# Kernel optimization log

Measured on AMD Instinct MI355X. Metric: run time of the kernel, lower is better.

## Reference

```python
import jax, jax.numpy as jnp
import numpy as np

S, B, D, H = 2048, 4, 1024, 16
HD = D // H  # 64
NEG = -1e9


def _rope_cache(seq_len, dim, base=10000.0):
    inv_freq = 1.0 / (base ** (jnp.arange(0, dim, 2, dtype=jnp.float32) / dim))
    pos = jnp.arange(seq_len, dtype=jnp.float32)
    freqs = jnp.einsum('i,j->ij', pos, inv_freq)          # [S, dim/2]
    emb = jnp.concatenate([freqs, freqs], axis=-1)         # [S, dim]
    return jnp.cos(emb)[None, None], jnp.sin(emb)[None, None]  # [1,1,S,dim]


def _apply_rotary(x, cos, sin):
    # rotated[..., ::2] = -x[..., 1::2]; rotated[..., 1::2] = x[..., ::2]
    x_even = x[..., ::2]
    x_odd = x[..., 1::2]
    rotated = jnp.stack([-x_odd, x_even], axis=-1).reshape(x.shape)
    return x * cos + rotated * sin


def setup_inputs() -> dict:
    key = jax.random.key(0)
    kx, kq, ko = jax.random.split(key, 3)
    x = jax.random.normal(kx, (S, B, D), dtype=jnp.float32)
    # additive causal mask, broadcastable over [B,H,S,S]
    causal = jnp.triu(jnp.full((S, S), NEG, dtype=jnp.float32), k=1)
    cos, sin = _rope_cache(S, HD)
    Wqkv = jax.random.normal(kq, (D, 3 * D), dtype=jnp.float32) * (D ** -0.5)
    Wout = jax.random.normal(ko, (D, D), dtype=jnp.float32) * (D ** -0.5)
    return {"x": x, "attn_mask": causal, "cos": cos, "sin": sin,
            "Wqkv": Wqkv, "Wout": Wout}


def reference(x, attn_mask, cos, sin, Wqkv, Wout):
    scale = 1.0 / jnp.sqrt(jnp.float32(HD))
    xb = jnp.swapaxes(x, 0, 1)                       # [B,S,D]
    qkv = jnp.einsum('bsd,de->bse', xb, Wqkv)        # [B,S,3D]
    q, k, v = jnp.split(qkv, 3, axis=-1)
    def heads(t):
        return t.reshape(B, S, H, HD).transpose(0, 2, 1, 3)  # [B,H,S,HD]
    q, k, v = heads(q), heads(k), heads(v)
    q = _apply_rotary(q, cos, sin)
    k = _apply_rotary(k, cos, sin)
    scores = jnp.einsum('bhsd,bhtd->bhst', q, k) * scale + attn_mask
    probs = jax.nn.softmax(scores, axis=-1)
    ctx = jnp.einsum('bhst,bhtd->bhsd', probs, v)
    ctx = ctx.transpose(0, 2, 1, 3).reshape(B, S, D)  # [B,S,D]
    out = jnp.einsum('bsd,de->bse', ctx, Wout)
    return jnp.swapaxes(out, 0, 1)                    # [S,B,D]
```

## Files before the change

kernel.cpp:

```cpp
#include <hip/hip_runtime.h>
#include <hip/hip_bf16.h>

#define S_LEN 2048
#define BATCH 4
#define DMODEL 1024
#define NHEAD 16
#define HDIM 64
#define E3 3072

typedef __bf16 bf16x8 __attribute__((ext_vector_type(8)));
typedef __bf16 bf16x4 __attribute__((ext_vector_type(4)));
typedef __bf16 bf16x2 __attribute__((ext_vector_type(2)));
typedef float f32x4 __attribute__((ext_vector_type(4)));

typedef const __attribute__((address_space(1))) void gvoid;
typedef __attribute__((address_space(3))) void lvoid;

__global__ void cast_f32_bf16(const float* __restrict__ src, __bf16* __restrict__ dst) {
    int i = (blockIdx.x * 256 + threadIdx.x) * 8;
    float4 a = *(const float4*)(src + i);
    float4 b = *(const float4*)(src + i + 4);
    bf16x8 v;
    v[0] = (__bf16)a.x; v[1] = (__bf16)a.y; v[2] = (__bf16)a.z; v[3] = (__bf16)a.w;
    v[4] = (__bf16)b.x; v[5] = (__bf16)b.y; v[6] = (__bf16)b.z; v[7] = (__bf16)b.w;
    *(bf16x8*)(dst + i) = v;
}

__global__ void transpose_f32_bf16(const float* __restrict__ src, __bf16* __restrict__ dst,
                                   int R, int C) {
    __shared__ float tile[32][33];
    int c0 = blockIdx.x * 32, r0 = blockIdx.y * 32;
    int tx = threadIdx.x, ty = threadIdx.y;
#pragma unroll
    for (int i = 0; i < 32; i += 8)
        tile[ty + i][tx] = src[(size_t)(r0 + ty + i) * C + c0 + tx];
    __syncthreads();
#pragma unroll
    for (int i = 0; i < 32; i += 8)
        dst[(size_t)(c0 + ty + i) * R + r0 + tx] = (__bf16)tile[tx][ty + i];
}

__global__ __launch_bounds__(256) void gemm_bt(
    const __bf16* __restrict__ A, const __bf16* __restrict__ BT, void* __restrict__ C,
    int K, int aSB, int aSS, int cSB, int cSS, int mode,
    const float* __restrict__ cosb, const float* __restrict__ sinb,
    __bf16* __restrict__ vtg) {
    __shared__ __bf16 lA[128 * 32];
    __shared__ __bf16 lB[128 * 32];

    const int tid = threadIdx.x;
    const int lane = tid & 63;
    const int quad = lane >> 4, l16 = lane & 15;
    const int wave = tid >> 6;
    const int wm = wave >> 1, wn = wave & 1;

    const int bid0 = blockIdx.y * gridDim.x + blockIdx.x;
    const int nwg = gridDim.x * gridDim.y;
    const int lid = (bid0 & 7) * (nwg >> 3) + (bid0 >> 3);
    const int bx = lid % gridDim.x;
    const int by = lid / gridDim.x;

    const int rm0 = by * 128;
    const int n0 = bx * 128;
    const int bb = rm0 / S_LEN;
    const int s0 = rm0 % S_LEN;

    const int lrow = lane >> 2;
    const int lch = (lane & 3) * 8;
    const int row0 = wave * 32;
    const __bf16* gA0 = A + (size_t)bb * aSB + (size_t)(s0 + row0 + lrow) * aSS + lch;
    const __bf16* gA1 = A + (size_t)bb * aSB + (size_t)(s0 + row0 + 16 + lrow) * aSS + lch;
    const __bf16* gB0 = BT + (size_t)(n0 + row0 + lrow) * K + lch;
    const __bf16* gB1 = BT + (size_t)(n0 + row0 + 16 + lrow) * K + lch;
    __bf16* ldsA0 = &lA[row0 * 32];
    __bf16* ldsA1 = &lA[(row0 + 16) * 32];
    __bf16* ldsB0 = &lB[row0 * 32];
    __bf16* ldsB1 = &lB[(row0 + 16) * 32];

    f32x4 acc[4][4];
#pragma unroll
    for (int i = 0; i < 4; i++)
#pragma unroll
        for (int j = 0; j < 4; j++) acc[i][j] = (f32x4){0.f, 0.f, 0.f, 0.f};

    for (int k0 = 0; k0 < K; k0 += 32) {
        __builtin_amdgcn_global_load_lds((gvoid*)(gA0 + k0), (lvoid*)ldsA0, 16, 0, 0);
        __builtin_amdgcn_global_load_lds((gvoid*)(gA1 + k0), (lvoid*)ldsA1, 16, 0, 0);
        __builtin_amdgcn_global_load_lds((gvoid*)(gB0 + k0), (lvoid*)ldsB0, 16, 0, 0);
        __builtin_amdgcn_global_load_lds((gvoid*)(gB1 + k0), (lvoid*)ldsB1, 16, 0, 0);
        __syncthreads();

        bf16x8 aF[4], bF[4];
#pragma unroll
        for (int i = 0; i < 4; i++) {
            aF[i] = *(const bf16x8*)&lA[(wm * 64 + i * 16 + l16) * 32 + quad * 8];
            bF[i] = *(const bf16x8*)&lB[(wn * 64 + i * 16 + l16) * 32 + quad * 8];
        }
#pragma unroll
        for (int i = 0; i < 4; i++)
#pragma unroll
            for (int j = 0; j < 4; j++)
                acc[i][j] = __builtin_amdgcn_mfma_f32_16x16x32_bf16(aF[i], bF[j], acc[i][j], 0, 0, 0);
        __syncthreads();
    }

    if (mode == 0) {
        if (n0 < 2048) {
#pragma unroll
            for (int i = 0; i < 4; i++) {
                const int rl = wm * 64 + i * 16 + quad * 4;
#pragma unroll
                for (int r = 0; r < 4; r++) {
                    const int s = s0 + rl + r;
                    const size_t rowOff = (size_t)bb * cSB + (size_t)s * cSS + n0 + wn * 64 + l16;
                    __bf16* cRow = (__bf16*)C + rowOff;
                    const float* cpr = cosb + s * HDIM;
                    const float* spr = sinb + s * HDIM;
#pragma unroll
                    for (int j = 0; j < 4; j++) {
                        float x = acc[i][j][r];
                        float y = __int_as_float(
                            __builtin_amdgcn_ds_swizzle(__float_as_int(x), 0x041F));
                        float c = cpr[j * 16 + l16];
                        float sn = spr[j * 16 + l16];
                        float out = (l16 & 1) ? fmaf(y, sn, x * c) : fmaf(-y, sn, x * c);
                        cRow[j * 16] = (__bf16)out;
                    }
                }
            }
        } else {
#pragma unroll
            for (int i = 0; i < 4; i++) {
                const int rl = wm * 64 + i * 16 + quad * 4;
#pragma unroll
                for (int j = 0; j < 4; j++) {
                    const int vcol = (n0 - 2048) + wn * 64 + j * 16 + l16;
                    const size_t vbase = ((size_t)(bb * 1024 + vcol)) * S_LEN + s0 + rl;
                    bf16x2 lo = {(__bf16)acc[i][j][0], (__bf16)acc[i][j][1]};
                    bf16x2 hi = {(__bf16)acc[i][j][2], (__bf16)acc[i][j][3]};
                    *(bf16x2*)(vtg + vbase) = lo;
                    *(bf16x2*)(vtg + vbase + 2) = hi;
                }
            }
        }
    } else {
#pragma unroll
        for (int i = 0; i < 4; i++) {
            const int rl = wm * 64 + i * 16 + quad * 4;
#pragma unroll
            for (int r = 0; r < 4; r++) {
                const size_t rowOff =
                    (size_t)bb * cSB + (size_t)(s0 + rl + r) * cSS + n0 + wn * 64 + l16;
                float* cRow = (float*)C + rowOff;
#pragma unroll
                for (int j = 0; j < 4; j++) cRow[j * 16] = acc[i][j][r];
            }
        }
    }
}

#define VT_IDX(hd, t) ((hd) * 72 + ((hd) >> 4) * 8 + (t))

__global__ __launch_bounds__(256) void attn_kernel(const __bf16* __restrict__ qkv,
                                                   const __bf16* __restrict__ vt,
                                                   __bf16* __restrict__ ctx) {
    __shared__ __bf16 sK[2][64 * 72];
    __shared__ __bf16 sVT[2][64 * 72 + 32];

    const int tid = threadIdx.x, lane = tid & 63, wave = tid >> 6;
    const int quad = lane >> 4, l16 = lane & 15;

    const int bid0 = blockIdx.y * 16 + blockIdx.x;
    const int lid = (bid0 & 7) * 128 + (bid0 >> 3);
    const int pair = lid & 15;
    const int bh = lid >> 4;
    const int b = bh >> 4, h = bh & 15;

    const int qtA = pair, qtB = 31 - pair;
    const int s0A = qtA * 64 + wave * 16;
    const int s0B = qtB * 64 + wave * 16;

    const int srow = tid >> 2;
    const int c0 = (tid & 3) * 16;

    const float qscale = 0.125f * 1.44269504f;
    const __bf16* kBase = qkv + (size_t)(b * S_LEN + srow) * E3 + DMODEL + h * HDIM + c0;
    const __bf16* vBase = vt + ((size_t)bh * HDIM + srow) * S_LEN + c0;

    const __bf16* qbA = qkv + (size_t)(b * S_LEN + s0A + l16) * E3 + h * HDIM;
    const __bf16* qbB = qkv + (size_t)(b * S_LEN + s0B + l16) * E3 + h * HDIM;
    bf16x8 qfA0 = *(const bf16x8*)(qbA + quad * 8);
    bf16x8 qfA1 = *(const bf16x8*)(qbA + 32 + quad * 8);
    bf16x8 qfB0 = *(const bf16x8*)(qbB + quad * 8);
    bf16x8 qfB1 = *(const bf16x8*)(qbB + 32 + quad * 8);
#pragma unroll
    for (int i = 0; i < 8; i++) {
        qfA0[i] = (__bf16)((float)qfA0[i] * qscale);
        qfA1[i] = (__bf16)((float)qfA1[i] * qscale);
        qfB0[i] = (__bf16)((float)qfB0[i] * qscale);
        qfB1[i] = (__bf16)((float)qfB1[i] * qscale);
    }

    f32x4 oA[4], oB[4], lacA, lacB;
#pragma unroll
    for (int j = 0; j < 4; j++) {
        oA[j] = (f32x4){0.f, 0.f, 0.f, 0.f};
        oB[j] = (f32x4){0.f, 0.f, 0.f, 0.f};
    }
    lacA = (f32x4){0.f, 0.f, 0.f, 0.f};
    lacB = (f32x4){0.f, 0.f, 0.f, 0.f};

    bf16x8 ones;
#pragma unroll
    for (int i = 0; i < 8; i++) ones[i] = (__bf16)1.0f;

    const __bf16* kRow = kBase;
    const __bf16* vRow = vBase;
    bf16x8 k0 = *(const bf16x8*)kRow;
    bf16x8 k1 = *(const bf16x8*)(kRow + 8);
    bf16x8 v0 = *(const bf16x8*)vRow;
    bf16x8 v1 = *(const bf16x8*)(vRow + 8);

    const int nT = qtB + 1;
#pragma unroll 1
    for (int it = 0; it < nT; ++it) {
        const int t0 = it * 64;
        __bf16* sKc = sK[it & 1];
        __bf16* sVc = sVT[it & 1];
        *(bf16x8*)&sKc[srow * 72 + c0] = k0;
        *(bf16x8*)&sKc[srow * 72 + c0 + 8] = k1;
        *(bf16x8*)&sVc[VT_IDX(srow, c0)] = v0;
        *(bf16x8*)&sVc[VT_IDX(srow, c0 + 8)] = v1;
        __syncthreads();

        if (it + 1 < nT) {
            kRow += (size_t)64 * E3;
            vRow += 64;
            k0 = *(const bf16x8*)kRow;
            k1 = *(const bf16x8*)(kRow + 8);
            v0 = *(const bf16x8*)vRow;
            v1 = *(const bf16x8*)(vRow + 8);
        }

        {
            f32x4 sc[4];
            __builtin_amdgcn_s_setprio(1);
#pragma unroll
            for (int jt = 0; jt < 4; jt++) {
                bf16x8 kf0 = *(const bf16x8*)&sKc[(jt * 16 + l16) * 72 + quad * 8];
                bf16x8 kf1 = *(const bf16x8*)&sKc[(jt * 16 + l16) * 72 + 32 + quad * 8];
                f32x4 z = (f32x4){0.f, 0.f, 0.f, 0.f};
                z = __builtin_amdgcn_mfma_f32_16x16x32_bf16(kf0, qfB0, z, 0, 0, 0);
                sc[jt] = __builtin_amdgcn_mfma_f32_16x16x32_bf16(kf1, qfB1, z, 0, 0, 0);
            }
            __builtin_amdgcn_s_setprio(0);

            float p[4][4];
            if (it == qtB) {
                const int qq = s0B + l16;
#pragma unroll
                for (int jt = 0; jt < 4; jt++)
#pragma unroll
                    for (int r = 0; r < 4; r++) {
                        int tt = t0 + jt * 16 + quad * 4 + r;
                        p[jt][r] = __builtin_exp2f((tt > qq) ? -1e9f : sc[jt][r]);
                    }
            } else {
#pragma unroll
                for (int jt = 0; jt < 4; jt++)
#pragma unroll
                    for (int r = 0; r < 4; r++) p[jt][r] = __builtin_exp2f(sc[jt][r]);
            }

            __builtin_amdgcn_s_setprio(1);
#pragma unroll
            for (int kt = 0; kt < 2; kt++) {
                bf16x8 pf;
#pragma unroll
                for (int r = 0; r < 4; r++) {
                    pf[r] = (__bf16)p[2 * kt][r];
                    pf[4 + r] = (__bf16)p[2 * kt + 1][r];
                }
#pragma unroll
                for (int jhd = 0; jhd < 4; jhd++) {
                    bf16x4 vlo = *(const bf16x4*)&sVc[VT_IDX(jhd * 16 + l16, kt * 32 + quad * 4)];
                    bf16x4 vhi = *(const bf16x4*)&sVc[VT_IDX(jhd * 16 + l16, kt * 32 + 16 + quad * 4)];
                    bf16x8 vf = __builtin_shufflevector(vlo, vhi, 0, 1, 2, 3, 4, 5, 6, 7);
                    oB[jhd] = __builtin_amdgcn_mfma_f32_16x16x32_bf16(pf, vf, oB[jhd], 0, 0, 0);
                }
                lacB = __builtin_amdgcn_mfma_f32_16x16x32_bf16(pf, ones, lacB, 0, 0, 0);
            }
            __builtin_amdgcn_s_setprio(0);
        }

        if (it <= qtA) {
            f32x4 sc[4];
            __builtin_amdgcn_s_setprio(1);
#pragma unroll
            for (int jt = 0; jt < 4; jt++) {
                bf16x8 kf0 = *(const bf16x8*)&sKc[(jt * 16 + l16) * 72 + quad * 8];
                bf16x8 kf1 = *(const bf16x8*)&sKc[(jt * 16 + l16) * 72 + 32 + quad * 8];
                f32x4 z = (f32x4){0.f, 0.f, 0.f, 0.f};
                z = __builtin_amdgcn_mfma_f32_16x16x32_bf16(kf0, qfA0, z, 0, 0, 0);
                sc[jt] = __builtin_amdgcn_mfma_f32_16x16x32_bf16(kf1, qfA1, z, 0, 0, 0);
            }
            __builtin_amdgcn_s_setprio(0);

            float p[4][4];
            if (it == qtA) {
                const int qq = s0A + l16;
#pragma unroll
                for (int jt = 0; jt < 4; jt++)
#pragma unroll
                    for (int r = 0; r < 4; r++) {
                        int tt = t0 + jt * 16 + quad * 4 + r;
                        p[jt][r] = __builtin_exp2f((tt > qq) ? -1e9f : sc[jt][r]);
                    }
            } else {
#pragma unroll
                for (int jt = 0; jt < 4; jt++)
#pragma unroll
                    for (int r = 0; r < 4; r++) p[jt][r] = __builtin_exp2f(sc[jt][r]);
            }

            __builtin_amdgcn_s_setprio(1);
#pragma unroll
            for (int kt = 0; kt < 2; kt++) {
                bf16x8 pf;
#pragma unroll
                for (int r = 0; r < 4; r++) {
                    pf[r] = (__bf16)p[2 * kt][r];
                    pf[4 + r] = (__bf16)p[2 * kt + 1][r];
                }
#pragma unroll
                for (int jhd = 0; jhd < 4; jhd++) {
                    bf16x4 vlo = *(const bf16x4*)&sVc[VT_IDX(jhd * 16 + l16, kt * 32 + quad * 4)];
                    bf16x4 vhi = *(const bf16x4*)&sVc[VT_IDX(jhd * 16 + l16, kt * 32 + 16 + quad * 4)];
                    bf16x8 vf = __builtin_shufflevector(vlo, vhi, 0, 1, 2, 3, 4, 5, 6, 7);
                    oA[jhd] = __builtin_amdgcn_mfma_f32_16x16x32_bf16(pf, vf, oA[jhd], 0, 0, 0);
                }
                lacA = __builtin_amdgcn_mfma_f32_16x16x32_bf16(pf, ones, lacA, 0, 0, 0);
            }
            __builtin_amdgcn_s_setprio(0);
        }
    }

#pragma unroll
    for (int r = 0; r < 4; r++) {
        float inv = 1.f / lacA[r];
        size_t crow = (size_t)(b * S_LEN + s0A + quad * 4 + r) * DMODEL + h * HDIM + l16;
#pragma unroll
        for (int j = 0; j < 4; j++) ctx[crow + j * 16] = (__bf16)(oA[j][r] * inv);
    }
#pragma unroll
    for (int r = 0; r < 4; r++) {
        float inv = 1.f / lacB[r];
        size_t crow = (size_t)(b * S_LEN + s0B + quad * 4 + r) * DMODEL + h * HDIM + l16;
#pragma unroll
        for (int j = 0; j < 4; j++) ctx[crow + j * 16] = (__bf16)(oB[j][r] * inv);
    }
}

extern "C" void kernel_launch(void* const* d_in, const int* in_sizes, int n_in,
                              void* d_out, int out_size, void* d_ws, size_t ws_size,
                              hipStream_t stream) {
    const float* x = (const float*)d_in[0];
    const float* cosb = (const float*)d_in[2];
    const float* sinb = (const float*)d_in[3];
    const float* Wqkv = (const float*)d_in[4];
    const float* Wout = (const float*)d_in[5];
    float* out = (float*)d_out;

    char* ws = (char*)d_ws;
    __bf16* qkv = (__bf16*)ws;
    __bf16* ctx = (__bf16*)(ws + 50331648);
    __bf16* WqkvT = (__bf16*)(ws + 50331648 + 16777216);
    __bf16* WoutT = (__bf16*)(ws + 50331648 + 16777216 + 6291456);
    __bf16* xb = ctx;
    __bf16* vtg = (__bf16*)d_out;

    cast_f32_bf16<<<(S_LEN * BATCH * DMODEL / 8) / 256, 256, 0, stream>>>(x, xb);
    transpose_f32_bf16<<<dim3(E3 / 32, DMODEL / 32), dim3(32, 8), 0, stream>>>(Wqkv, WqkvT, DMODEL, E3);
    transpose_f32_bf16<<<dim3(DMODEL / 32, DMODEL / 32), dim3(32, 8), 0, stream>>>(Wout, WoutT, DMODEL, DMODEL);

    gemm_bt<<<dim3(E3 / 128, (BATCH * S_LEN) / 128), 256, 0, stream>>>(
        xb, WqkvT, qkv, DMODEL,
        DMODEL, BATCH * DMODEL,
        S_LEN * E3, E3, 0, cosb, sinb, vtg);

    attn_kernel<<<dim3(16, BATCH * NHEAD), 256, 0, stream>>>(qkv, vtg, ctx);

    gemm_bt<<<dim3(DMODEL / 128, (BATCH * S_LEN) / 128), 256, 0, stream>>>(
        ctx, WoutT, out, DMODEL,
        S_LEN * DMODEL, DMODEL,
        DMODEL, BATCH * DMODEL, 1, nullptr, nullptr, nullptr);
}
```

Before: 301.9 us.

## Replace 128x128 GEMM with double-buffered 256x256 tile, K=64 swizzled LDS

```diff
diff --git a/kernel.cpp b/kernel.cpp
--- a/kernel.cpp
+++ b/kernel.cpp
@@ -40,19 +40,20 @@
         dst[(size_t)(c0 + ty + i) * R + r0 + tx] = (__bf16)tile[tx][ty + i];
 }
 
-__global__ __launch_bounds__(256) void gemm_bt(
+__global__ __launch_bounds__(512) void gemm256(
     const __bf16* __restrict__ A, const __bf16* __restrict__ BT, void* __restrict__ C,
     int K, int aSB, int aSS, int cSB, int cSS, int mode,
     const float* __restrict__ cosb, const float* __restrict__ sinb,
     __bf16* __restrict__ vtg) {
-    __shared__ __bf16 lA[128 * 32];
-    __shared__ __bf16 lB[128 * 32];
+    __shared__ __bf16 lA[2][16384];
+    __shared__ __bf16 lB[2][16384];
 
     const int tid = threadIdx.x;
     const int lane = tid & 63;
-    const int quad = lane >> 4, l16 = lane & 15;
+    const int quad = (lane >> 4) & 3, l16 = lane & 15;
     const int wave = tid >> 6;
-    const int wm = wave >> 1, wn = wave & 1;
+    const int wm = wave >> 2;
+    const int wn = wave & 3;
 
     const int bid0 = blockIdx.y * gridDim.x + blockIdx.x;
     const int nwg = gridDim.x * gridDim.y;
@@ -60,100 +61,146 @@
     const int bx = lid % gridDim.x;
     const int by = lid / gridDim.x;
 
-    const int rm0 = by * 128;
-    const int n0 = bx * 128;
+    const int rm0 = by * 256;
+    const int n0 = bx * 256;
     const int bb = rm0 / S_LEN;
     const int s0 = rm0 % S_LEN;
 
-    const int lrow = lane >> 2;
-    const int lch = (lane & 3) * 8;
-    const int row0 = wave * 32;
-    const __bf16* gA0 = A + (size_t)bb * aSB + (size_t)(s0 + row0 + lrow) * aSS + lch;
-    const __bf16* gA1 = A + (size_t)bb * aSB + (size_t)(s0 + row0 + 16 + lrow) * aSS + lch;
-    const __bf16* gB0 = BT + (size_t)(n0 + row0 + lrow) * K + lch;
-    const __bf16* gB1 = BT + (size_t)(n0 + row0 + 16 + lrow) * K + lch;
-    __bf16* ldsA0 = &lA[row0 * 32];
-    __bf16* ldsA1 = &lA[(row0 + 16) * 32];
-    __bf16* ldsB0 = &lB[row0 * 32];
-    __bf16* ldsB1 = &lB[(row0 + 16) * 32];
-
-    f32x4 acc[4][4];
-#pragma unroll
-    for (int i = 0; i < 4; i++)
+    const int srow = tid >> 3;
+    const int scs = ((tid & 7) ^ (srow & 7)) * 8;
+    const __bf16* gA = A + (size_t)bb * aSB + (size_t)(s0 + srow) * aSS + scs;
+    const __bf16* gB = BT + (size_t)(n0 + srow) * K + scs;
+    const int ldsOff = wave * 512;
+
+    f32x4 acc[8][4];
+#pragma unroll
+    for (int i = 0; i < 8; i++)
 #pragma unroll
         for (int j = 0; j < 4; j++) acc[i][j] = (f32x4){0.f, 0.f, 0.f, 0.f};
 
-    for (int k0 = 0; k0 < K; k0 += 32) {
-        __builtin_amdgcn_global_load_lds((gvoid*)(gA0 + k0), (lvoid*)ldsA0, 16, 0, 0);
-        __builtin_amdgcn_global_load_lds((gvoid*)(gA1 + k0), (lvoid*)ldsA1, 16, 0, 0);
-        __builtin_amdgcn_global_load_lds((gvoid*)(gB0 + k0), (lvoid*)ldsB0, 16, 0, 0);
-        __builtin_amdgcn_global_load_lds((gvoid*)(gB1 + k0), (lvoid*)ldsB1, 16, 0, 0);
-        __syncthreads();
-
-        bf16x8 aF[4], bF[4];
-#pragma unroll
-        for (int i = 0; i < 4; i++) {
-            aF[i] = *(const bf16x8*)&lA[(wm * 64 + i * 16 + l16) * 32 + quad * 8];
-            bF[i] = *(const bf16x8*)&lB[(wn * 64 + i * 16 + l16) * 32 + quad * 8];
-        }
-#pragma unroll
-        for (int i = 0; i < 4; i++)
-#pragma unroll
-            for (int j = 0; j < 4; j++)
-                acc[i][j] = __builtin_amdgcn_mfma_f32_16x16x32_bf16(aF[i], bF[j], acc[i][j], 0, 0, 0);
-        __syncthreads();
+#pragma unroll
+    for (int h = 0; h < 2; h++) {
+        __builtin_amdgcn_global_load_lds((gvoid*)(gA + (size_t)(h * 128) * aSS),
+                                         (lvoid*)&lA[0][h * 8192 + ldsOff], 16, 0, 0);
+        __builtin_amdgcn_global_load_lds((gvoid*)(gA + (size_t)(h * 128 + 64) * aSS),
+                                         (lvoid*)&lA[0][h * 8192 + 4096 + ldsOff], 16, 0, 0);
+        __builtin_amdgcn_global_load_lds((gvoid*)(gB + (size_t)(h * 128) * K),
+                                         (lvoid*)&lB[0][h * 8192 + ldsOff], 16, 0, 0);
+        __builtin_amdgcn_global_load_lds((gvoid*)(gB + (size_t)(h * 128 + 64) * K),
+                                         (lvoid*)&lB[0][h * 8192 + 4096 + ldsOff], 16, 0, 0);
+    }
+
+    const int nT = K >> 6;
+#pragma unroll 1
+    for (int t = 0; t < nT; ++t) {
+        asm volatile("s_waitcnt vmcnt(0)" ::: "memory");
+        __builtin_amdgcn_s_barrier();
+        asm volatile("" ::: "memory");
+        __builtin_amdgcn_sched_barrier(0);
+
+        const int cur = t & 1;
+        const int kn = (t + 1) << 6;
+        const bool more = (t + 1 < nT);
+        const __bf16* lAc = lA[cur];
+        const __bf16* lBc = lB[cur];
+
+        bf16x8 bfr[4][2];
+#pragma unroll
+        for (int p = 0; p < 4; ++p) {
+            if (more) {
+                if (p < 2) {
+                    const __bf16* g = gA + (size_t)(p * 128) * aSS + kn;
+                    __builtin_amdgcn_global_load_lds(
+                        (gvoid*)g, (lvoid*)&lA[cur ^ 1][p * 8192 + ldsOff], 16, 0, 0);
+                    __builtin_amdgcn_global_load_lds(
+                        (gvoid*)(g + (size_t)64 * aSS),
+                        (lvoid*)&lA[cur ^ 1][p * 8192 + 4096 + ldsOff], 16, 0, 0);
+                } else {
+                    const __bf16* g = gB + (size_t)((p - 2) * 128) * K + kn;
+                    __builtin_amdgcn_global_load_lds(
+                        (gvoid*)g, (lvoid*)&lB[cur ^ 1][(p - 2) * 8192 + ldsOff], 16, 0, 0);
+                    __builtin_amdgcn_global_load_lds(
+                        (gvoid*)(g + (size_t)64 * K),
+                        (lvoid*)&lB[cur ^ 1][(p - 2) * 8192 + 4096 + ldsOff], 16, 0, 0);
+                }
+            }
+            if (p == 0) {
+#pragma unroll
+                for (int nf = 0; nf < 4; nf++)
+#pragma unroll
+                    for (int kh = 0; kh < 2; kh++)
+                        bfr[nf][kh] = *(const bf16x8*)&lBc[(wn >> 1) * 8192 +
+                                                           ((wn & 1) * 64 + nf * 16 + l16) * 64 +
+                                                           (((kh * 4 + quad) ^ (l16 & 7)) * 8)];
+            }
+            bf16x8 afr[2][2];
+#pragma unroll
+            for (int m2 = 0; m2 < 2; m2++)
+#pragma unroll
+                for (int kh = 0; kh < 2; kh++)
+                    afr[m2][kh] = *(const bf16x8*)&lAc[wm * 8192 +
+                                                       ((p * 2 + m2) * 16 + l16) * 64 +
+                                                       (((kh * 4 + quad) ^ (l16 & 7)) * 8)];
+            __builtin_amdgcn_s_setprio(1);
+#pragma unroll
+            for (int m2 = 0; m2 < 2; m2++)
+#pragma unroll
+                for (int nf = 0; nf < 4; nf++) {
+                    f32x4 a = acc[p * 2 + m2][nf];
+                    a = __builtin_amdgcn_mfma_f32_16x16x32_bf16(afr[m2][0], bfr[nf][0], a, 0, 0, 0);
+                    a = __builtin_amdgcn_mfma_f32_16x16x32_bf16(afr[m2][1], bfr[nf][1], a, 0, 0, 0);
+                    acc[p * 2 + m2][nf] = a;
+                }
+            __builtin_amdgcn_s_setprio(0);
+        }
     }
 
     if (mode == 0) {
         if (n0 < 2048) {
 #pragma unroll
-            for (int i = 0; i < 4; i++) {
-                const int rl = wm * 64 + i * 16 + quad * 4;
+            for (int mf = 0; mf < 8; mf++) {
 #pragma unroll
                 for (int r = 0; r < 4; r++) {
-                    const int s = s0 + rl + r;
-                    const size_t rowOff = (size_t)bb * cSB + (size_t)s * cSS + n0 + wn * 64 + l16;
-                    __bf16* cRow = (__bf16*)C + rowOff;
+                    const int s = s0 + wm * 128 + mf * 16 + quad * 4 + r;
+                    __bf16* cRow =
+                        (__bf16*)C + (size_t)bb * cSB + (size_t)s * cSS + n0 + wn * 64 + l16;
                     const float* cpr = cosb + s * HDIM;
                     const float* spr = sinb + s * HDIM;
 #pragma unroll
-                    for (int j = 0; j < 4; j++) {
-                        float x = acc[i][j][r];
+                    for (int nf = 0; nf < 4; nf++) {
+                        float x = acc[mf][nf][r];
                         float y = __int_as_float(
                             __builtin_amdgcn_ds_swizzle(__float_as_int(x), 0x041F));
-                        float c = cpr[j * 16 + l16];
-                        float sn = spr[j * 16 + l16];
+                        float c = cpr[nf * 16 + l16];
+                        float sn = spr[nf * 16 + l16];
                         float out = (l16 & 1) ? fmaf(y, sn, x * c) : fmaf(-y, sn, x * c);
-                        cRow[j * 16] = (__bf16)out;
+                        cRow[nf * 16] = (__bf16)out;
                     }
                 }
             }
         } else {
 #pragma unroll
-            for (int i = 0; i < 4; i++) {
-                const int rl = wm * 64 + i * 16 + quad * 4;
-#pragma unroll
-                for (int j = 0; j < 4; j++) {
-                    const int vcol = (n0 - 2048) + wn * 64 + j * 16 + l16;
-                    const size_t vbase = ((size_t)(bb * 1024 + vcol)) * S_LEN + s0 + rl;
-                    bf16x2 lo = {(__bf16)acc[i][j][0], (__bf16)acc[i][j][1]};
-                    bf16x2 hi = {(__bf16)acc[i][j][2], (__bf16)acc[i][j][3]};
+            for (int mf = 0; mf < 8; mf++)
+#pragma unroll
+                for (int nf = 0; nf < 4; nf++) {
+                    const int vcol = (n0 - 2048) + wn * 64 + nf * 16 + l16;
+                    const size_t vbase =
+                        ((size_t)(bb * 1024 + vcol)) * S_LEN + s0 + wm * 128 + mf * 16 + quad * 4;
+                    bf16x2 lo = {(__bf16)acc[mf][nf][0], (__bf16)acc[mf][nf][1]};
+                    bf16x2 hi = {(__bf16)acc[mf][nf][2], (__bf16)acc[mf][nf][3]};
                     *(bf16x2*)(vtg + vbase) = lo;
                     *(bf16x2*)(vtg + vbase + 2) = hi;
                 }
-            }
         }
     } else {
 #pragma unroll
-        for (int i = 0; i < 4; i++) {
-            const int rl = wm * 64 + i * 16 + quad * 4;
+        for (int mf = 0; mf < 8; mf++) {
 #pragma unroll
             for (int r = 0; r < 4; r++) {
-                const size_t rowOff =
-                    (size_t)bb * cSB + (size_t)(s0 + rl + r) * cSS + n0 + wn * 64 + l16;
-                float* cRow = (float*)C + rowOff;
-#pragma unroll
-                for (int j = 0; j < 4; j++) cRow[j * 16] = acc[i][j][r];
+                const int s = s0 + wm * 128 + mf * 16 + quad * 4 + r;
+                float* cRow = (float*)C + (size_t)bb * cSB + (size_t)s * cSS + n0 + wn * 64 + l16;
+#pragma unroll
+                for (int nf = 0; nf < 4; nf++) cRow[nf * 16] = acc[mf][nf][r];
             }
         }
     }
@@ -383,14 +430,14 @@
     transpose_f32_bf16<<<dim3(E3 / 32, DMODEL / 32), dim3(32, 8), 0, stream>>>(Wqkv, WqkvT, DMODEL, E3);
     transpose_f32_bf16<<<dim3(DMODEL / 32, DMODEL / 32), dim3(32, 8), 0, stream>>>(Wout, WoutT, DMODEL, DMODEL);
 
-    gemm_bt<<<dim3(E3 / 128, (BATCH * S_LEN) / 128), 256, 0, stream>>>(
+    gemm256<<<dim3(E3 / 256, (BATCH * S_LEN) / 256), 512, 0, stream>>>(
         xb, WqkvT, qkv, DMODEL,
         DMODEL, BATCH * DMODEL,
         S_LEN * E3, E3, 0, cosb, sinb, vtg);
 
     attn_kernel<<<dim3(16, BATCH * NHEAD), 256, 0, stream>>>(qkv, vtg, ctx);
 
-    gemm_bt<<<dim3(DMODEL / 128, (BATCH * S_LEN) / 128), 256, 0, stream>>>(
+    gemm256<<<dim3(DMODEL / 256, (BATCH * S_LEN) / 256), 512, 0, stream>>>(
         ctx, WoutT, out, DMODEL,
         S_LEN * DMODEL, DMODEL,
         DMODEL, BATCH * DMODEL, 1, nullptr, nullptr, nullptr);
```

Measured after the change: 323.7 us. 1.07x slower.
